# Performance work log

Measured on AMD Instinct MI355X. Metric: run time of the kernel, lower is better.

Reference implementation:

```python
import jax, jax.numpy as jnp
import numpy as np

# geomloss SamplesLoss('sinkhorn', p=2, blur=0.05, scaling=0.5, debias=True) math
P = 2
BLUR = 0.05
SCALING = 0.5
DIAMETER = 64.0  # static conservative bound on point-cloud diameter for randn D=64 data


def _eps_schedule():
    eps_list = []
    e = DIAMETER ** P
    target = BLUR ** P
    while e > target:
        eps_list.append(e)
        e *= SCALING ** P
    eps_list.append(target)
    return np.array(eps_list, dtype=np.float32)


def _cost(x, y):
    # C_ij = ||x_i - y_j||^2 / 2   (p=2 cost of geomloss)
    sq = (jnp.sum(x * x, -1)[:, :, None] * 0.5
          + jnp.sum(y * y, -1)[:, None, :] * 0.5
          - jnp.einsum('bnd,bmd->bnm', x, y))
    return jnp.maximum(sq, 0.0)


def _softmin(eps, C, h):
    # f_i = -eps * log sum_j exp(h_j - C_ij / eps);  C: (B,N,M), h: (B,M)
    return -eps * jax.nn.logsumexp(h[:, None, :] - C / eps, axis=-1)


def setup_inputs() -> dict:
    key = jax.random.key(0)
    k1, k2, k3, k4 = jax.random.split(key, 4)
    B, N, M, D = 8, 2048, 2048, 64
    x = jax.random.normal(k1, (B, N, D), dtype=jnp.float32)
    y = jax.random.normal(k2, (B, M, D), dtype=jnp.float32)
    w1 = jax.random.uniform(k3, (B, N), dtype=jnp.float32) + 0.01
    w2 = jax.random.uniform(k4, (B, M), dtype=jnp.float32) + 0.01
    w1 = w1 / jnp.sum(w1, axis=-1, keepdims=True)
    w2 = w2 / jnp.sum(w2, axis=-1, keepdims=True)
    return {'x': x, 'y': y, 'w1': w1, 'w2': w2}


def _sinkhorn_divergence(x, y, w1, w2):
    a_log = jnp.log(w1)
    b_log = jnp.log(w2)
    eps_list = jnp.asarray(_eps_schedule())

    # --- Sinkhorn loop on detached quantities (geomloss detaches the loop) ---
    xd = jax.lax.stop_gradient(x)
    yd = jax.lax.stop_gradient(y)
    ald = jax.lax.stop_gradient(a_log)
    bld = jax.lax.stop_gradient(b_log)
    C_xy_d = _cost(xd, yd)
    C_yx_d = jnp.swapaxes(C_xy_d, 1, 2)
    C_xx_d = _cost(xd, xd)
    C_yy_d = _cost(yd, yd)

    eps0 = eps_list[0]
    f_ab = _softmin(eps0, C_xy_d, bld)
    g_ba = _softmin(eps0, C_yx_d, ald)
    f_aa = _softmin(eps0, C_xx_d, ald)
    g_bb = _softmin(eps0, C_yy_d, bld)

    def step(carry, eps):
        f_ab, g_ba, f_aa, g_bb = carry
        ft = _softmin(eps, C_xy_d, bld + g_ba / eps)
        gt = _softmin(eps, C_yx_d, ald + f_ab / eps)
        f_aa_t = _softmin(eps, C_xx_d, ald + f_aa / eps)
        g_bb_t = _softmin(eps, C_yy_d, bld + g_bb / eps)
        return (0.5 * (f_ab + ft), 0.5 * (g_ba + gt),
                0.5 * (f_aa + f_aa_t), 0.5 * (g_bb + g_bb_t)), None

    (f_ab, g_ba, f_aa, g_bb), _ = jax.lax.scan(step, (f_ab, g_ba, f_aa, g_bb), eps_list)

    # --- last extrapolation at eps = blur^p, differentiable ---
    eps = eps_list[-1]
    C_xy = _cost(x, y)
    C_yx = jnp.swapaxes(C_xy, 1, 2)
    C_xx = _cost(x, x)
    C_yy = _cost(y, y)
    f_ab_f = _softmin(eps, C_xy, b_log + g_ba / eps)
    g_ba_f = _softmin(eps, C_yx, a_log + f_ab / eps)
    f_aa_f = _softmin(eps, C_xx, a_log + f_aa / eps)
    g_bb_f = _softmin(eps, C_yy, b_log + g_bb / eps)

    # debiased sinkhorn cost per batch element
    loss = (jnp.sum(w1 * (f_ab_f - f_aa_f), axis=-1)
            + jnp.sum(w2 * (g_ba_f - g_bb_f), axis=-1))
    return loss


def reference(x, y, w1, w2):
    loss = _sinkhorn_divergence(x, y, w1, w2)
    return jnp.mean(loss)  # reduction='mean'
```

## Files before the change

kernel.cpp:

```cpp
#include <hip/hip_runtime.h>

#define NB 8
#define NN 2048
#define MM 2048
#define DD 64
#define NMAT ((size_t)NN * (size_t)MM)
#define NCHK 16
#define TS 128

#define CSCALE 320.0f
#define CDEC   (1.0f / CSCALE)

typedef _Float16 half_t;
typedef __attribute__((ext_vector_type(8))) _Float16 f16x8;
typedef __attribute__((ext_vector_type(4))) float f32x4;

__device__ unsigned short g_C[3 * NB * NMAT];
__device__ half_t g_xh[NB * NN * DD];
__device__ half_t g_yh[NB * MM * DD];
__device__ float g_fab[3][NB * NN], g_gba[3][NB * NN];
__device__ float g_faa[3][NB * NN], g_gbb[3][NB * NN];
__device__ float g_alog[NB * NN], g_blog[NB * NN];
__device__ float g_xn[NB * NN], g_yn[NB * NN];
__device__ float g_h0[NB * MM], g_h1[NB * NN], g_h2[NB * NN], g_h3[NB * MM];
__device__ float2 g_pfab[NB * NCHK * NN];
__device__ float2 g_pgba[NB * NCHK * NN];
__device__ float2 g_pfaa[NB * NCHK * NN];
__device__ float2 g_pgbb[NB * NCHK * NN];

__global__ __launch_bounds__(256) void prep_kernel(
    const float* __restrict__ x, const float* __restrict__ y,
    const float* __restrict__ w1, const float* __restrict__ w2)
{
  int gid = blockIdx.x * 256 + threadIdx.x;
  if (gid < NB * NN) {
    g_alog[gid] = logf(w1[gid]);
    g_blog[gid] = logf(w2[gid]);
  }
  int lane = threadIdx.x & 63;
  int row = blockIdx.x * 4 + (threadIdx.x >> 6);
  float xv = x[(size_t)row * DD + lane];
  float yv = y[(size_t)row * DD + lane];
  g_xh[(size_t)row * DD + lane] = (half_t)xv;
  g_yh[(size_t)row * DD + lane] = (half_t)yv;
  float sx = xv * xv;
  float sy = yv * yv;
#pragma unroll
  for (int off = 32; off > 0; off >>= 1) {
    sx += __shfl_down(sx, off);
    sy += __shfl_down(sy, off);
  }
  if (lane == 0) {
    g_xn[row] = 0.5f * sx;
    g_yn[row] = 0.5f * sy;
  }
}

__global__ __launch_bounds__(256) void cost_mfma()
{
  const int slab = blockIdx.z >> 3;
  const int b = blockIdx.z & 7;
  int I, J;
  if (slab) {
    if (blockIdx.x >= 136) return;
    int rem = blockIdx.x, ii = 0;
    while (rem >= NCHK - ii) { rem -= NCHK - ii; ++ii; }
    I = ii; J = ii + rem;
  } else {
    I = blockIdx.x >> 4;
    J = blockIdx.x & 15;
  }

  const half_t* Ah = (slab == 2) ? g_yh : g_xh;
  const half_t* Bh = (slab == 0) ? g_yh : ((slab == 1) ? g_xh : g_yh);
  const float* na = (slab == 2) ? g_yn : g_xn;
  const float* nbp = (slab == 0) ? g_yn : ((slab == 1) ? g_xn : g_yn);
  unsigned short* Cout = g_C + (size_t)slab * NB * NMAT + (size_t)b * NMAT;

  const int t = threadIdx.x;
  const int w = t >> 6, lane = t & 63;
  const int m = lane & 15, quad = lane >> 4;
  const int i0 = I * TS, j0 = J * TS;

  const half_t* Abase = Ah + ((size_t)b * NN + i0 + 32 * w + m) * DD + quad * 8;
  const half_t* Bbase = Bh + ((size_t)b * MM + j0 + m) * DD + quad * 8;

  f32x4 acc[2][8];
#pragma unroll
  for (int g = 0; g < 2; ++g)
#pragma unroll
    for (int c = 0; c < 8; ++c) acc[g][c] = (f32x4){0.f, 0.f, 0.f, 0.f};

#pragma unroll
  for (int s = 0; s < 2; ++s) {
    f16x8 a0 = *(const f16x8*)(Abase + s * 32);
    f16x8 a1 = *(const f16x8*)(Abase + (size_t)16 * DD + s * 32);
#pragma unroll
    for (int c = 0; c < 8; ++c) {
      f16x8 bf = *(const f16x8*)(Bbase + (size_t)(16 * c) * DD + s * 32);
      acc[0][c] = __builtin_amdgcn_mfma_f32_16x16x32_f16(a0, bf, acc[0][c], 0, 0, 0);
      acc[1][c] = __builtin_amdgcn_mfma_f32_16x16x32_f16(a1, bf, acc[1][c], 0, 0, 0);
    }
  }

  __shared__ unsigned short tile[TS * TS];
  float4 xr[2];
#pragma unroll
  for (int g = 0; g < 2; ++g)
    xr[g] = *(const float4*)(na + b * NN + i0 + 32 * w + 16 * g + 4 * quad);
#pragma unroll
  for (int c = 0; c < 8; ++c) {
    float yv = nbp[b * MM + j0 + 16 * c + m];
#pragma unroll
    for (int g = 0; g < 2; ++g) {
      float xg[4] = {xr[g].x, xr[g].y, xr[g].z, xr[g].w};
#pragma unroll
      for (int r = 0; r < 4; ++r) {
        float cv = fmaxf(xg[r] + yv - acc[g][c][r], 0.f);
        unsigned int u = __float2uint_rn(fminf(cv * CSCALE, 65535.f));
        tile[(32 * w + 16 * g + 4 * quad + r) * TS + 16 * c + m] = (unsigned short)u;
      }
    }
  }
  __syncthreads();

  const uint4* tl = (const uint4*)tile;
#pragma unroll
  for (int p = 0; p < 8; ++p) {
    int u = p * 256 + t;
    int row = u >> 4, c8 = (u & 15) * 8;
    *(uint4*)(Cout + (size_t)(i0 + row) * MM + j0 + c8) = tl[u];
  }
}

__global__ __launch_bounds__(256) void hprep_kernel(
    const float* __restrict__ fab_in, const float* __restrict__ gba_in,
    const float* __restrict__ faa_in, const float* __restrict__ gbb_in,
    float gs)
{
  int i = blockIdx.x * 256 + threadIdx.x;
  g_h0[i] = fmaf(gs, gba_in[i], g_blog[i]);
  g_h1[i] = fmaf(gs, fab_in[i], g_alog[i]);
  g_h2[i] = fmaf(gs, faa_in[i], g_alog[i]);
  g_h3[i] = fmaf(gs, gbb_in[i], g_blog[i]);
}

struct TileArgs {
  const unsigned short* C;
  const float* hrow;
  const float* hcol;
  float2* prow;
  float2* pcol;
  int sym;
};

__global__ __launch_bounds__(256) void tile_pass(
    TileArgs T0, TileArgs T1, TileArgs T2, float inv_eps)
{
  TileArgs A = (blockIdx.z == 0) ? T0 : (blockIdx.z == 1) ? T1 : T2;
  int I, J;
  if (A.sym) {
    if (blockIdx.x >= 136) return;
    int rem = blockIdx.x, ii = 0;
    while (rem >= NCHK - ii) { rem -= NCHK - ii; ++ii; }
    I = ii; J = ii + rem;
  } else {
    I = blockIdx.x >> 4;
    J = blockIdx.x & 15;
  }
  const int b = blockIdx.y;
  const int t = threadIdx.x;
  const int ctr = t & 15;
  const int rtr = t >> 4;
  const float csneg = -inv_eps * CDEC;

  const unsigned short* Cb = A.C + (size_t)b * NMAT
                           + (size_t)(I * TS) * MM + J * TS;

  float hr[8], hc[8];
  {
    const float* hrp = A.hrow + (size_t)b * MM + J * TS + ctr * 8;
    const float* hcp = A.hcol + (size_t)b * MM + I * TS + rtr * 8;
#pragma unroll
    for (int k = 0; k < 8; ++k) { hr[k] = hrp[k]; hc[k] = hcp[k]; }
  }

  uint4 cu[8];
#pragma unroll
  for (int r8 = 0; r8 < 8; ++r8)
    cu[r8] = *(const uint4*)(Cb + (size_t)(rtr * 8 + r8) * MM + ctr * 8);

  __shared__ float redR[TS][17], redC[TS][17];
  __shared__ float rowM[TS], colM[TS];

  float rm[8], cm[8];
#pragma unroll
  for (int k = 0; k < 8; ++k) { rm[k] = -3.0e38f; cm[k] = -3.0e38f; }
#pragma unroll
  for (int r8 = 0; r8 < 8; ++r8) {
    float base[8];
    base[0] = (float)(cu[r8].x & 0xffff) * csneg;
    base[1] = (float)(cu[r8].x >> 16)    * csneg;
    base[2] = (float)(cu[r8].y & 0xffff) * csneg;
    base[3] = (float)(cu[r8].y >> 16)    * csneg;
    base[4] = (float)(cu[r8].z & 0xffff) * csneg;
    base[5] = (float)(cu[r8].z >> 16)    * csneg;
    base[6] = (float)(cu[r8].w & 0xffff) * csneg;
    base[7] = (float)(cu[r8].w >> 16)    * csneg;
#pragma unroll
    for (int c8 = 0; c8 < 8; ++c8) {
      rm[r8] = fmaxf(rm[r8], hr[c8] + base[c8]);
      cm[c8] = fmaxf(cm[c8], hc[r8] + base[c8]);
    }
  }
#pragma unroll
  for (int r8 = 0; r8 < 8; ++r8) redR[rtr * 8 + r8][ctr] = rm[r8];
#pragma unroll
  for (int c8 = 0; c8 < 8; ++c8) redC[ctr * 8 + c8][rtr] = cm[c8];
  __syncthreads();
  if (t < TS) {
    float m = redR[t][0];
#pragma unroll
    for (int k = 1; k < 16; ++k) m = fmaxf(m, redR[t][k]);
    rowM[t] = m;
  } else {
    int tt = t - TS;
    float m = redC[tt][0];
#pragma unroll
    for (int k = 1; k < 16; ++k) m = fmaxf(m, redC[tt][k]);
    colM[tt] = m;
  }
  __syncthreads();

  float rmv[8], cmv[8];
#pragma unroll
  for (int k = 0; k < 8; ++k) {
    rmv[k] = rowM[rtr * 8 + k];
    cmv[k] = colM[ctr * 8 + k];
  }

  float rs[8], cs[8];
#pragma unroll
  for (int k = 0; k < 8; ++k) { rs[k] = 0.f; cs[k] = 0.f; }
#pragma unroll
  for (int r8 = 0; r8 < 8; ++r8) {
    float base[8];
    base[0] = (float)(cu[r8].x & 0xffff) * csneg;
    base[1] = (float)(cu[r8].x >> 16)    * csneg;
    base[2] = (float)(cu[r8].y & 0xffff) * csneg;
    base[3] = (float)(cu[r8].y >> 16)    * csneg;
    base[4] = (float)(cu[r8].z & 0xffff) * csneg;
    base[5] = (float)(cu[r8].z >> 16)    * csneg;
    base[6] = (float)(cu[r8].w & 0xffff) * csneg;
    base[7] = (float)(cu[r8].w >> 16)    * csneg;
#pragma unroll
    for (int c8 = 0; c8 < 8; ++c8) {
      rs[r8] += __expf(hr[c8] + base[c8] - rmv[r8]);
      cs[c8] += __expf(hc[r8] + base[c8] - cmv[c8]);
    }
  }
#pragma unroll
  for (int r8 = 0; r8 < 8; ++r8) redR[rtr * 8 + r8][ctr] = rs[r8];
#pragma unroll
  for (int c8 = 0; c8 < 8; ++c8) redC[ctr * 8 + c8][rtr] = cs[c8];
  __syncthreads();
  if (t < TS) {
    float s = 0.f;
#pragma unroll
    for (int k = 0; k < 16; ++k) s += redR[t][k];
    A.prow[((size_t)b * NCHK + J) * NN + I * TS + t] = make_float2(rowM[t], s);
  } else {
    int tt = t - TS;
    if (!(A.sym && I == J)) {
      float s = 0.f;
#pragma unroll
      for (int k = 0; k < 16; ++k) s += redC[tt][k];
      A.pcol[((size_t)b * NCHK + I) * NN + J * TS + tt] = make_float2(colM[tt], s);
    }
  }
}

struct MergeArgs {
  const float2* part;
  const float* fold;
  float* fout;
  const float* hbase;
  float* hout;
};

__global__ __launch_bounds__(256) void merge4(
    MergeArgs M0, MergeArgs M1, MergeArgs M2, MergeArgs M3,
    float eps, float alpha, float beta, float nextgs)
{
  MergeArgs A = (blockIdx.z == 0) ? M0 : (blockIdx.z == 1) ? M1
              : (blockIdx.z == 2) ? M2 : M3;
  const int b = blockIdx.y;
  const int i = blockIdx.x * 256 + threadIdx.x;
  float2 p[NCHK];
#pragma unroll
  for (int k = 0; k < NCHK; ++k)
    p[k] = A.part[((size_t)b * NCHK + k) * NN + i];
  float M = p[0].x;
#pragma unroll
  for (int k = 1; k < NCHK; ++k) M = fmaxf(M, p[k].x);
  float S = 0.f;
#pragma unroll
  for (int k = 0; k < NCHK; ++k) S += p[k].y * __expf(p[k].x - M);
  float ft = -eps * (M + __logf(S));
  int idx = b * NN + i;
  float fnew = alpha * A.fold[idx] + beta * ft;
  A.fout[idx] = fnew;
  A.hout[idx] = fmaf(nextgs, fnew, A.hbase[idx]);
}

__global__ __launch_bounds__(256) void loss_kernel(
    const float* __restrict__ w1, const float* __restrict__ w2,
    float* __restrict__ out)
{
  __shared__ float red[256];
  float acc = 0.f;
  for (int idx = threadIdx.x; idx < NB * NN; idx += 256) {
    acc += w1[idx] * (g_fab[2][idx] - g_faa[2][idx])
         + w2[idx] * (g_gba[2][idx] - g_gbb[2][idx]);
  }
  red[threadIdx.x] = acc;
  __syncthreads();
  for (int s = 128; s > 0; s >>= 1) {
    if (threadIdx.x < s) red[threadIdx.x] += red[threadIdx.x + s];
    __syncthreads();
  }
  if (threadIdx.x == 0) out[0] = red[0] * (1.0f / NB);
}

extern "C" void kernel_launch(void* const* d_in, const int* in_sizes, int n_in,
                              void* d_out, int out_size, void* d_ws, size_t ws_size,
                              hipStream_t stream)
{
  const float* x = (const float*)d_in[0];
  const float* y = (const float*)d_in[1];
  const float* w1 = (const float*)d_in[2];
  const float* w2 = (const float*)d_in[3];
  float* out = (float*)d_out;

  unsigned short* Cbase;
  hipGetSymbolAddress((void**)&Cbase, HIP_SYMBOL(g_C));
  unsigned short* Cxy = Cbase + 0ull * NB * NMAT;
  unsigned short* Cxx = Cbase + 1ull * NB * NMAT;
  unsigned short* Cyy = Cbase + 2ull * NB * NMAT;
  float *h0, *h1, *h2, *h3, *fabp, *gbap, *faap, *gbbp, *alog, *blog;
  float2 *pfab, *pgba, *pfaa, *pgbb;
  hipGetSymbolAddress((void**)&h0, HIP_SYMBOL(g_h0));
  hipGetSymbolAddress((void**)&h1, HIP_SYMBOL(g_h1));
  hipGetSymbolAddress((void**)&h2, HIP_SYMBOL(g_h2));
  hipGetSymbolAddress((void**)&h3, HIP_SYMBOL(g_h3));
  hipGetSymbolAddress((void**)&fabp, HIP_SYMBOL(g_fab));
  hipGetSymbolAddress((void**)&gbap, HIP_SYMBOL(g_gba));
  hipGetSymbolAddress((void**)&faap, HIP_SYMBOL(g_faa));
  hipGetSymbolAddress((void**)&gbbp, HIP_SYMBOL(g_gbb));
  hipGetSymbolAddress((void**)&alog, HIP_SYMBOL(g_alog));
  hipGetSymbolAddress((void**)&blog, HIP_SYMBOL(g_blog));
  hipGetSymbolAddress((void**)&pfab, HIP_SYMBOL(g_pfab));
  hipGetSymbolAddress((void**)&pgba, HIP_SYMBOL(g_pgba));
  hipGetSymbolAddress((void**)&pfaa, HIP_SYMBOL(g_pfaa));
  hipGetSymbolAddress((void**)&pgbb, HIP_SYMBOL(g_pgbb));

  auto fab = [&](int s) { return fabp + (size_t)s * NB * NN; };
  auto gba = [&](int s) { return gbap + (size_t)s * NB * NN; };
  auto faa = [&](int s) { return faap + (size_t)s * NB * NN; };
  auto gbb = [&](int s) { return gbbp + (size_t)s * NB * NN; };

  float eps_list[32];
  int ne = 0;
  {
    double v = 64.0 * 64.0;
    double tgt = 0.05 * 0.05;
    while (v > tgt) { eps_list[ne++] = (float)v; v *= 0.25; }
    eps_list[ne++] = (float)tgt;
  }

  prep_kernel<<<4096, 256, 0, stream>>>(x, y, w1, w2);

  cost_mfma<<<dim3(256, 1, 24), 256, 0, stream>>>();

  dim3 tg(256, NB, 3);
  dim3 mg(NN / 256, NB, 4);

  auto launch_iter = [&](float eps, float alpha, float beta, float nextgs,
                         int in, int outsel) {
    float inv = 1.0f / eps;
    TileArgs T0 = {Cxy, h0, h1, pfab, pgba, 0};
    TileArgs T1 = {Cxx, h2, h2, pfaa, pfaa, 1};
    TileArgs T2 = {Cyy, h3, h3, pgbb, pgbb, 1};
    tile_pass<<<tg, 256, 0, stream>>>(T0, T1, T2, inv);
    MergeArgs M0 = {pfab, fab(in), fab(outsel), alog, h1};
    MergeArgs M1 = {pgba, gba(in), gba(outsel), blog, h0};
    MergeArgs M2 = {pfaa, faa(in), faa(outsel), alog, h2};
    MergeArgs M3 = {pgbb, gbb(in), gbb(outsel), blog, h3};
    merge4<<<mg, 256, 0, stream>>>(M0, M1, M2, M3, eps, alpha, beta, nextgs);
  };

  hprep_kernel<<<64, 256, 0, stream>>>(fab(0), gba(0), faa(0), gbb(0), 0.f);
  launch_iter(eps_list[0], 0.f, 1.f, 1.0f / eps_list[0], 0, 0);

  int cur = 0;
  for (int k = 0; k < ne; ++k) {
    int nxt = 1 - cur;
    float nextgs = 1.0f / ((k < ne - 1) ? eps_list[k + 1] : eps_list[ne - 1]);
    launch_iter(eps_list[k], 0.5f, 0.5f, nextgs, cur, nxt);
    cur = nxt;
  }

  launch_iter(eps_list[ne - 1], 0.f, 1.f, 0.f, cur, 2);

  loss_kernel<<<1, 256, 0, stream>>>(w1, w2, out);
}
```

Before: 711.9 us.

## Recompute cost tiles on the fly with MFMA inside tile pass instead of storing

Removes the precomputed 16-bit quantized cost matrices and the separate cost kernel. Each tile_pass block now recomputes its 128x128 tile of x·y dot products with f16 MFMA and folds the squared norms and potentials into per-row and per-column offsets for the logsumexp. This swaps the large per-iteration reads of the stored cost matrix for extra MFMA work and small reads of the f16 point clouds. It also drops the 320x quantization of costs, which changes precision, and the clamp of negative costs to zero is no longer applied.

```diff
diff --git a/kernel.cpp b/kernel.cpp
--- a/kernel.cpp
+++ b/kernel.cpp
@@ -8,14 +8,10 @@
 #define NCHK 16
 #define TS 128
 
-#define CSCALE 320.0f
-#define CDEC   (1.0f / CSCALE)
-
 typedef _Float16 half_t;
 typedef __attribute__((ext_vector_type(8))) _Float16 f16x8;
 typedef __attribute__((ext_vector_type(4))) float f32x4;
 
-__device__ unsigned short g_C[3 * NB * NMAT];
 __device__ half_t g_xh[NB * NN * DD];
 __device__ half_t g_yh[NB * MM * DD];
 __device__ float g_fab[3][NB * NN], g_gba[3][NB * NN];
@@ -56,83 +52,6 @@
   }
 }
 
-__global__ __launch_bounds__(256) void cost_mfma()
-{
-  const int slab = blockIdx.z >> 3;
-  const int b = blockIdx.z & 7;
-  int I, J;
-  if (slab) {
-    if (blockIdx.x >= 136) return;
-    int rem = blockIdx.x, ii = 0;
-    while (rem >= NCHK - ii) { rem -= NCHK - ii; ++ii; }
-    I = ii; J = ii + rem;
-  } else {
-    I = blockIdx.x >> 4;
-    J = blockIdx.x & 15;
-  }
-
-  const half_t* Ah = (slab == 2) ? g_yh : g_xh;
-  const half_t* Bh = (slab == 0) ? g_yh : ((slab == 1) ? g_xh : g_yh);
-  const float* na = (slab == 2) ? g_yn : g_xn;
-  const float* nbp = (slab == 0) ? g_yn : ((slab == 1) ? g_xn : g_yn);
-  unsigned short* Cout = g_C + (size_t)slab * NB * NMAT + (size_t)b * NMAT;
-
-  const int t = threadIdx.x;
-  const int w = t >> 6, lane = t & 63;
-  const int m = lane & 15, quad = lane >> 4;
-  const int i0 = I * TS, j0 = J * TS;
-
-  const half_t* Abase = Ah + ((size_t)b * NN + i0 + 32 * w + m) * DD + quad * 8;
-  const half_t* Bbase = Bh + ((size_t)b * MM + j0 + m) * DD + quad * 8;
-
-  f32x4 acc[2][8];
-#pragma unroll
-  for (int g = 0; g < 2; ++g)
-#pragma unroll
-    for (int c = 0; c < 8; ++c) acc[g][c] = (f32x4){0.f, 0.f, 0.f, 0.f};
-
-#pragma unroll
-  for (int s = 0; s < 2; ++s) {
-    f16x8 a0 = *(const f16x8*)(Abase + s * 32);
-    f16x8 a1 = *(const f16x8*)(Abase + (size_t)16 * DD + s * 32);
-#pragma unroll
-    for (int c = 0; c < 8; ++c) {
-      f16x8 bf = *(const f16x8*)(Bbase + (size_t)(16 * c) * DD + s * 32);
-      acc[0][c] = __builtin_amdgcn_mfma_f32_16x16x32_f16(a0, bf, acc[0][c], 0, 0, 0);
-      acc[1][c] = __builtin_amdgcn_mfma_f32_16x16x32_f16(a1, bf, acc[1][c], 0, 0, 0);
-    }
-  }
-
-  __shared__ unsigned short tile[TS * TS];
-  float4 xr[2];
-#pragma unroll
-  for (int g = 0; g < 2; ++g)
-    xr[g] = *(const float4*)(na + b * NN + i0 + 32 * w + 16 * g + 4 * quad);
-#pragma unroll
-  for (int c = 0; c < 8; ++c) {
-    float yv = nbp[b * MM + j0 + 16 * c + m];
-#pragma unroll
-    for (int g = 0; g < 2; ++g) {
-      float xg[4] = {xr[g].x, xr[g].y, xr[g].z, xr[g].w};
-#pragma unroll
-      for (int r = 0; r < 4; ++r) {
-        float cv = fmaxf(xg[r] + yv - acc[g][c][r], 0.f);
-        unsigned int u = __float2uint_rn(fminf(cv * CSCALE, 65535.f));
-        tile[(32 * w + 16 * g + 4 * quad + r) * TS + 16 * c + m] = (unsigned short)u;
-      }
-    }
-  }
-  __syncthreads();
-
-  const uint4* tl = (const uint4*)tile;
-#pragma unroll
-  for (int p = 0; p < 8; ++p) {
-    int u = p * 256 + t;
-    int row = u >> 4, c8 = (u & 15) * 8;
-    *(uint4*)(Cout + (size_t)(i0 + row) * MM + j0 + c8) = tl[u];
-  }
-}
-
 __global__ __launch_bounds__(256) void hprep_kernel(
     const float* __restrict__ fab_in, const float* __restrict__ gba_in,
     const float* __restrict__ faa_in, const float* __restrict__ gbb_in,
@@ -145,8 +64,11 @@
   g_h3[i] = fmaf(gs, gbb_in[i], g_blog[i]);
 }
 
-struct TileArgs {
-  const unsigned short* C;
+struct TPArgs {
+  const half_t* Ar;
+  const half_t* Bc;
+  const float* nrow;
+  const float* ncol;
   const float* hrow;
   const float* hcol;
   float2* prow;
@@ -155,9 +77,9 @@
 };
 
 __global__ __launch_bounds__(256) void tile_pass(
-    TileArgs T0, TileArgs T1, TileArgs T2, float inv_eps)
-{
-  TileArgs A = (blockIdx.z == 0) ? T0 : (blockIdx.z == 1) ? T1 : T2;
+    TPArgs T0, TPArgs T1, TPArgs T2, float inv_eps)
+{
+  TPArgs A = (blockIdx.z == 0) ? T0 : (blockIdx.z == 1) ? T1 : T2;
   int I, J;
   if (A.sym) {
     if (blockIdx.x >= 136) return;
@@ -170,25 +92,54 @@
   }
   const int b = blockIdx.y;
   const int t = threadIdx.x;
-  const int ctr = t & 15;
-  const int rtr = t >> 4;
-  const float csneg = -inv_eps * CDEC;
-
-  const unsigned short* Cb = A.C + (size_t)b * NMAT
-                           + (size_t)(I * TS) * MM + J * TS;
-
-  float hr[8], hc[8];
-  {
-    const float* hrp = A.hrow + (size_t)b * MM + J * TS + ctr * 8;
-    const float* hcp = A.hcol + (size_t)b * MM + I * TS + rtr * 8;
-#pragma unroll
-    for (int k = 0; k < 8; ++k) { hr[k] = hrp[k]; hc[k] = hcp[k]; }
-  }
-
-  uint4 cu[8];
-#pragma unroll
-  for (int r8 = 0; r8 < 8; ++r8)
-    cu[r8] = *(const uint4*)(Cb + (size_t)(rtr * 8 + r8) * MM + ctr * 8);
+  const int w = t >> 6, lane = t & 63;
+  const int m = lane & 15, quad = lane >> 4;
+  const int i0 = I * TS, j0 = J * TS;
+  const float ie = inv_eps;
+
+  const half_t* Abase = A.Ar + ((size_t)b * NN + i0 + 32 * w + m) * DD + quad * 8;
+  const half_t* Bbase = A.Bc + ((size_t)b * MM + j0 + m) * DD + quad * 8;
+
+  f32x4 acc[2][8];
+#pragma unroll
+  for (int g = 0; g < 2; ++g)
+#pragma unroll
+    for (int c = 0; c < 8; ++c) acc[g][c] = (f32x4){0.f, 0.f, 0.f, 0.f};
+
+#pragma unroll
+  for (int s = 0; s < 2; ++s) {
+    f16x8 a0 = *(const f16x8*)(Abase + s * 32);
+    f16x8 a1 = *(const f16x8*)(Abase + (size_t)16 * DD + s * 32);
+#pragma unroll
+    for (int c = 0; c < 8; ++c) {
+      f16x8 bf = *(const f16x8*)(Bbase + (size_t)(16 * c) * DD + s * 32);
+      acc[0][c] = __builtin_amdgcn_mfma_f32_16x16x32_f16(a0, bf, acc[0][c], 0, 0, 0);
+      acc[1][c] = __builtin_amdgcn_mfma_f32_16x16x32_f16(a1, bf, acc[1][c], 0, 0, 0);
+    }
+  }
+
+  float Aj[8], Bj[8];
+  float Ai[8], Bi[8];
+#pragma unroll
+  for (int c = 0; c < 8; ++c) {
+    int j = b * MM + j0 + 16 * c + m;
+    float ynj = A.ncol[j];
+    Bj[c] = -ynj * ie;
+    Aj[c] = A.hrow[j] + Bj[c];
+  }
+#pragma unroll
+  for (int g = 0; g < 2; ++g) {
+    int ib = b * NN + i0 + 32 * w + 16 * g + 4 * quad;
+    float4 xn4 = *(const float4*)(A.nrow + ib);
+    float4 hc4 = *(const float4*)(A.hcol + ib);
+    float xg[4] = {xn4.x, xn4.y, xn4.z, xn4.w};
+    float hg[4] = {hc4.x, hc4.y, hc4.z, hc4.w};
+#pragma unroll
+    for (int r = 0; r < 4; ++r) {
+      Bi[g * 4 + r] = -xg[r] * ie;
+      Ai[g * 4 + r] = hg[r] + Bi[g * 4 + r];
+    }
+  }
 
   __shared__ float redR[TS][17], redC[TS][17];
   __shared__ float rowM[TS], colM[TS];
@@ -197,72 +148,69 @@
 #pragma unroll
   for (int k = 0; k < 8; ++k) { rm[k] = -3.0e38f; cm[k] = -3.0e38f; }
 #pragma unroll
-  for (int r8 = 0; r8 < 8; ++r8) {
-    float base[8];
-    base[0] = (float)(cu[r8].x & 0xffff) * csneg;
-    base[1] = (float)(cu[r8].x >> 16)    * csneg;
-    base[2] = (float)(cu[r8].y & 0xffff) * csneg;
-    base[3] = (float)(cu[r8].y >> 16)    * csneg;
-    base[4] = (float)(cu[r8].z & 0xffff) * csneg;
-    base[5] = (float)(cu[r8].z >> 16)    * csneg;
-    base[6] = (float)(cu[r8].w & 0xffff) * csneg;
-    base[7] = (float)(cu[r8].w >> 16)    * csneg;
-#pragma unroll
-    for (int c8 = 0; c8 < 8; ++c8) {
-      rm[r8] = fmaxf(rm[r8], hr[c8] + base[c8]);
-      cm[c8] = fmaxf(cm[c8], hc[r8] + base[c8]);
-    }
-  }
-#pragma unroll
-  for (int r8 = 0; r8 < 8; ++r8) redR[rtr * 8 + r8][ctr] = rm[r8];
-#pragma unroll
-  for (int c8 = 0; c8 < 8; ++c8) redC[ctr * 8 + c8][rtr] = cm[c8];
+  for (int g = 0; g < 2; ++g)
+#pragma unroll
+    for (int c = 0; c < 8; ++c) {
+      f32x4 tv = acc[g][c];
+#pragma unroll
+      for (int r = 0; r < 4; ++r) {
+        float tt = tv[r] * ie;
+        tv[r] = tt;
+        rm[g * 4 + r] = fmaxf(rm[g * 4 + r], tt + Bi[g * 4 + r] + Aj[c]);
+        cm[c] = fmaxf(cm[c], tt + Ai[g * 4 + r] + Bj[c]);
+      }
+      acc[g][c] = tv;
+    }
+#pragma unroll
+  for (int k = 0; k < 8; ++k)
+    redR[32 * w + 16 * (k >> 2) + 4 * quad + (k & 3)][m] = rm[k];
+#pragma unroll
+  for (int c = 0; c < 8; ++c)
+    redC[16 * c + m][w * 4 + quad] = cm[c];
   __syncthreads();
   if (t < TS) {
-    float m = redR[t][0];
-#pragma unroll
-    for (int k = 1; k < 16; ++k) m = fmaxf(m, redR[t][k]);
-    rowM[t] = m;
+    float v = redR[t][0];
+#pragma unroll
+    for (int k = 1; k < 16; ++k) v = fmaxf(v, redR[t][k]);
+    rowM[t] = v;
   } else {
     int tt = t - TS;
-    float m = redC[tt][0];
-#pragma unroll
-    for (int k = 1; k < 16; ++k) m = fmaxf(m, redC[tt][k]);
-    colM[tt] = m;
-  }
-  __syncthreads();
-
-  float rmv[8], cmv[8];
-#pragma unroll
-  for (int k = 0; k < 8; ++k) {
-    rmv[k] = rowM[rtr * 8 + k];
-    cmv[k] = colM[ctr * 8 + k];
-  }
+    float v = redC[tt][0];
+#pragma unroll
+    for (int k = 1; k < 16; ++k) v = fmaxf(v, redC[tt][k]);
+    colM[tt] = v;
+  }
+  __syncthreads();
+
+  float BR[8], CB[8];
+#pragma unroll
+  for (int k = 0; k < 8; ++k)
+    BR[k] = Bi[k] - rowM[32 * w + 16 * (k >> 2) + 4 * quad + (k & 3)];
+#pragma unroll
+  for (int c = 0; c < 8; ++c)
+    CB[c] = Bj[c] - colM[16 * c + m];
 
   float rs[8], cs[8];
 #pragma unroll
   for (int k = 0; k < 8; ++k) { rs[k] = 0.f; cs[k] = 0.f; }
 #pragma unroll
-  for (int r8 = 0; r8 < 8; ++r8) {
-    float base[8];
-    base[0] = (float)(cu[r8].x & 0xffff) * csneg;
-    base[1] = (float)(cu[r8].x >> 16)    * csneg;
-    base[2] = (float)(cu[r8].y & 0xffff) * csneg;
-    base[3] = (float)(cu[r8].y >> 16)    * csneg;
-    base[4] = (float)(cu[r8].z & 0xffff) * csneg;
-    base[5] = (float)(cu[r8].z >> 16)    * csneg;
-    base[6] = (float)(cu[r8].w & 0xffff) * csneg;
-    base[7] = (float)(cu[r8].w >> 16)    * csneg;
-#pragma unroll
-    for (int c8 = 0; c8 < 8; ++c8) {
-      rs[r8] += __expf(hr[c8] + base[c8] - rmv[r8]);
-      cs[c8] += __expf(hc[r8] + base[c8] - cmv[c8]);
-    }
-  }
-#pragma unroll
-  for (int r8 = 0; r8 < 8; ++r8) redR[rtr * 8 + r8][ctr] = rs[r8];
-#pragma unroll
-  for (int c8 = 0; c8 < 8; ++c8) redC[ctr * 8 + c8][rtr] = cs[c8];
+  for (int g = 0; g < 2; ++g)
+#pragma unroll
+    for (int c = 0; c < 8; ++c) {
+      f32x4 tv = acc[g][c];
+#pragma unroll
+      for (int r = 0; r < 4; ++r) {
+        rs[g * 4 + r] += __expf(tv[r] + BR[g * 4 + r] + Aj[c]);
+        cs[c] += __expf(tv[r] + Ai[g * 4 + r] + CB[c]);
+      }
+    }
+  __syncthreads();
+#pragma unroll
+  for (int k = 0; k < 8; ++k)
+    redR[32 * w + 16 * (k >> 2) + 4 * quad + (k & 3)][m] = rs[k];
+#pragma unroll
+  for (int c = 0; c < 8; ++c)
+    redC[16 * c + m][w * 4 + quad] = cs[c];
   __syncthreads();
   if (t < TS) {
     float s = 0.f;
@@ -342,13 +290,13 @@
   const float* w2 = (const float*)d_in[3];
   float* out = (float*)d_out;
 
-  unsigned short* Cbase;
-  hipGetSymbolAddress((void**)&Cbase, HIP_SYMBOL(g_C));
-  unsigned short* Cxy = Cbase + 0ull * NB * NMAT;
-  unsigned short* Cxx = Cbase + 1ull * NB * NMAT;
-  unsigned short* Cyy = Cbase + 2ull * NB * NMAT;
-  float *h0, *h1, *h2, *h3, *fabp, *gbap, *faap, *gbbp, *alog, *blog;
+  half_t *xh, *yh;
+  float *xn, *yn, *h0, *h1, *h2, *h3, *fabp, *gbap, *faap, *gbbp, *alog, *blog;
   float2 *pfab, *pgba, *pfaa, *pgbb;
+  hipGetSymbolAddress((void**)&xh, HIP_SYMBOL(g_xh));
+  hipGetSymbolAddress((void**)&yh, HIP_SYMBOL(g_yh));
+  hipGetSymbolAddress((void**)&xn, HIP_SYMBOL(g_xn));
+  hipGetSymbolAddress((void**)&yn, HIP_SYMBOL(g_yn));
   hipGetSymbolAddress((void**)&h0, HIP_SYMBOL(g_h0));
   hipGetSymbolAddress((void**)&h1, HIP_SYMBOL(g_h1));
   hipGetSymbolAddress((void**)&h2, HIP_SYMBOL(g_h2));
@@ -380,17 +328,15 @@
 
   prep_kernel<<<4096, 256, 0, stream>>>(x, y, w1, w2);
 
-  cost_mfma<<<dim3(256, 1, 24), 256, 0, stream>>>();
-
   dim3 tg(256, NB, 3);
   dim3 mg(NN / 256, NB, 4);
 
   auto launch_iter = [&](float eps, float alpha, float beta, float nextgs,
                          int in, int outsel) {
     float inv = 1.0f / eps;
-    TileArgs T0 = {Cxy, h0, h1, pfab, pgba, 0};
-    TileArgs T1 = {Cxx, h2, h2, pfaa, pfaa, 1};
-    TileArgs T2 = {Cyy, h3, h3, pgbb, pgbb, 1};
+    TPArgs T0 = {xh, yh, xn, yn, h0, h1, pfab, pgba, 0};
+    TPArgs T1 = {xh, xh, xn, xn, h2, h2, pfaa, pfaa, 1};
+    TPArgs T2 = {yh, yh, yn, yn, h3, h3, pgbb, pgbb, 1};
     tile_pass<<<tg, 256, 0, stream>>>(T0, T1, T2, inv);
     MergeArgs M0 = {pfab, fab(in), fab(outsel), alog, h1};
     MergeArgs M1 = {pgba, gba(in), gba(outsel), blog, h0};
```

Measured after the change: 1.655 ms. 132% more time.

## Use base-2 exponent domain and wavefront shuffles for row reductions in tile pass

Applied to the files above, without the earlier changes.

Pre-scales the potentials and cost scale by log2(e), so each logit is a single FMA and the raw hardware exp2 and log2 builtins replace __expf/__logf. The merge kernel is adjusted to work in the base-2 domain and converts back with ln2. Row max and row sum reductions now use xor-shuffles within the 16 lanes that share a row instead of a shared-memory transpose, which drops the redR array and some LDS traffic. The column reduction still goes through shared memory and gains an extra barrier. It relies on the 16 lanes of a row group sitting in the same wavefront.

```diff
diff --git a/kernel.cpp b/kernel.cpp
--- a/kernel.cpp
+++ b/kernel.cpp
@@ -10,6 +10,8 @@
 
 #define CSCALE 320.0f
 #define CDEC   (1.0f / CSCALE)
+#define LOG2E  1.4426950408889634f
+#define LN2    0.6931471805599453f
 
 typedef _Float16 half_t;
 typedef __attribute__((ext_vector_type(8))) _Float16 f16x8;
@@ -172,17 +174,20 @@
   const int t = threadIdx.x;
   const int ctr = t & 15;
   const int rtr = t >> 4;
-  const float csneg = -inv_eps * CDEC;
+  const float cs2 = -inv_eps * CDEC * LOG2E;
 
   const unsigned short* Cb = A.C + (size_t)b * NMAT
                            + (size_t)(I * TS) * MM + J * TS;
 
-  float hr[8], hc[8];
+  float hr2[8], hc2[8];
   {
     const float* hrp = A.hrow + (size_t)b * MM + J * TS + ctr * 8;
     const float* hcp = A.hcol + (size_t)b * MM + I * TS + rtr * 8;
 #pragma unroll
-    for (int k = 0; k < 8; ++k) { hr[k] = hrp[k]; hc[k] = hcp[k]; }
+    for (int k = 0; k < 8; ++k) {
+      hr2[k] = hrp[k] * LOG2E;
+      hc2[k] = hcp[k] * LOG2E;
+    }
   }
 
   uint4 cu[8];
@@ -190,93 +195,86 @@
   for (int r8 = 0; r8 < 8; ++r8)
     cu[r8] = *(const uint4*)(Cb + (size_t)(rtr * 8 + r8) * MM + ctr * 8);
 
-  __shared__ float redR[TS][17], redC[TS][17];
-  __shared__ float rowM[TS], colM[TS];
+  __shared__ float redC[TS][17];
+  __shared__ float colM[TS];
 
   float rm[8], cm[8];
 #pragma unroll
   for (int k = 0; k < 8; ++k) { rm[k] = -3.0e38f; cm[k] = -3.0e38f; }
 #pragma unroll
   for (int r8 = 0; r8 < 8; ++r8) {
-    float base[8];
-    base[0] = (float)(cu[r8].x & 0xffff) * csneg;
-    base[1] = (float)(cu[r8].x >> 16)    * csneg;
-    base[2] = (float)(cu[r8].y & 0xffff) * csneg;
-    base[3] = (float)(cu[r8].y >> 16)    * csneg;
-    base[4] = (float)(cu[r8].z & 0xffff) * csneg;
-    base[5] = (float)(cu[r8].z >> 16)    * csneg;
-    base[6] = (float)(cu[r8].w & 0xffff) * csneg;
-    base[7] = (float)(cu[r8].w >> 16)    * csneg;
+    float u[8];
+    u[0] = (float)(cu[r8].x & 0xffff);
+    u[1] = (float)(cu[r8].x >> 16);
+    u[2] = (float)(cu[r8].y & 0xffff);
+    u[3] = (float)(cu[r8].y >> 16);
+    u[4] = (float)(cu[r8].z & 0xffff);
+    u[5] = (float)(cu[r8].z >> 16);
+    u[6] = (float)(cu[r8].w & 0xffff);
+    u[7] = (float)(cu[r8].w >> 16);
 #pragma unroll
     for (int c8 = 0; c8 < 8; ++c8) {
-      rm[r8] = fmaxf(rm[r8], hr[c8] + base[c8]);
-      cm[c8] = fmaxf(cm[c8], hc[r8] + base[c8]);
+      rm[r8] = fmaxf(rm[r8], fmaf(u[c8], cs2, hr2[c8]));
+      cm[c8] = fmaxf(cm[c8], fmaf(u[c8], cs2, hc2[r8]));
     }
   }
 #pragma unroll
-  for (int r8 = 0; r8 < 8; ++r8) redR[rtr * 8 + r8][ctr] = rm[r8];
+  for (int mask = 1; mask < 16; mask <<= 1)
+#pragma unroll
+    for (int k = 0; k < 8; ++k)
+      rm[k] = fmaxf(rm[k], __shfl_xor(rm[k], mask));
 #pragma unroll
   for (int c8 = 0; c8 < 8; ++c8) redC[ctr * 8 + c8][rtr] = cm[c8];
   __syncthreads();
   if (t < TS) {
-    float m = redR[t][0];
-#pragma unroll
-    for (int k = 1; k < 16; ++k) m = fmaxf(m, redR[t][k]);
-    rowM[t] = m;
-  } else {
-    int tt = t - TS;
-    float m = redC[tt][0];
-#pragma unroll
-    for (int k = 1; k < 16; ++k) m = fmaxf(m, redC[tt][k]);
-    colM[tt] = m;
-  }
-  __syncthreads();
-
-  float rmv[8], cmv[8];
-#pragma unroll
-  for (int k = 0; k < 8; ++k) {
-    rmv[k] = rowM[rtr * 8 + k];
-    cmv[k] = colM[ctr * 8 + k];
-  }
+    float m = redC[t][0];
+#pragma unroll
+    for (int k = 1; k < 16; ++k) m = fmaxf(m, redC[t][k]);
+    colM[t] = m;
+  }
+  __syncthreads();
+  float cmv[8];
+#pragma unroll
+  for (int c8 = 0; c8 < 8; ++c8) cmv[c8] = colM[ctr * 8 + c8];
 
   float rs[8], cs[8];
 #pragma unroll
   for (int k = 0; k < 8; ++k) { rs[k] = 0.f; cs[k] = 0.f; }
 #pragma unroll
   for (int r8 = 0; r8 < 8; ++r8) {
-    float base[8];
-    base[0] = (float)(cu[r8].x & 0xffff) * csneg;
-    base[1] = (float)(cu[r8].x >> 16)    * csneg;
-    base[2] = (float)(cu[r8].y & 0xffff) * csneg;
-    base[3] = (float)(cu[r8].y >> 16)    * csneg;
-    base[4] = (float)(cu[r8].z & 0xffff) * csneg;
-    base[5] = (float)(cu[r8].z >> 16)    * csneg;
-    base[6] = (float)(cu[r8].w & 0xffff) * csneg;
-    base[7] = (float)(cu[r8].w >> 16)    * csneg;
+    float u[8];
+    u[0] = (float)(cu[r8].x & 0xffff);
+    u[1] = (float)(cu[r8].x >> 16);
+    u[2] = (float)(cu[r8].y & 0xffff);
+    u[3] = (float)(cu[r8].y >> 16);
+    u[4] = (float)(cu[r8].z & 0xffff);
+    u[5] = (float)(cu[r8].z >> 16);
+    u[6] = (float)(cu[r8].w & 0xffff);
+    u[7] = (float)(cu[r8].w >> 16);
 #pragma unroll
     for (int c8 = 0; c8 < 8; ++c8) {
-      rs[r8] += __expf(hr[c8] + base[c8] - rmv[r8]);
-      cs[c8] += __expf(hc[r8] + base[c8] - cmv[c8]);
+      rs[r8] += __builtin_amdgcn_exp2f(fmaf(u[c8], cs2, hr2[c8]) - rm[r8]);
+      cs[c8] += __builtin_amdgcn_exp2f(fmaf(u[c8], cs2, hc2[r8]) - cmv[c8]);
     }
   }
 #pragma unroll
-  for (int r8 = 0; r8 < 8; ++r8) redR[rtr * 8 + r8][ctr] = rs[r8];
+  for (int mask = 1; mask < 16; mask <<= 1)
+#pragma unroll
+    for (int k = 0; k < 8; ++k)
+      rs[k] += __shfl_xor(rs[k], mask);
+  if (ctr < 8) {
+    A.prow[((size_t)b * NCHK + J) * NN + I * TS + rtr * 8 + ctr]
+        = make_float2(rm[ctr], rs[ctr]);
+  }
+  __syncthreads();
 #pragma unroll
   for (int c8 = 0; c8 < 8; ++c8) redC[ctr * 8 + c8][rtr] = cs[c8];
   __syncthreads();
-  if (t < TS) {
+  if (t < TS && !(A.sym && I == J)) {
     float s = 0.f;
 #pragma unroll
-    for (int k = 0; k < 16; ++k) s += redR[t][k];
-    A.prow[((size_t)b * NCHK + J) * NN + I * TS + t] = make_float2(rowM[t], s);
-  } else {
-    int tt = t - TS;
-    if (!(A.sym && I == J)) {
-      float s = 0.f;
-#pragma unroll
-      for (int k = 0; k < 16; ++k) s += redC[tt][k];
-      A.pcol[((size_t)b * NCHK + I) * NN + J * TS + tt] = make_float2(colM[tt], s);
-    }
+    for (int k = 0; k < 16; ++k) s += redC[t][k];
+    A.pcol[((size_t)b * NCHK + I) * NN + J * TS + t] = make_float2(colM[t], s);
   }
 }
 
@@ -305,8 +303,9 @@
   for (int k = 1; k < NCHK; ++k) M = fmaxf(M, p[k].x);
   float S = 0.f;
 #pragma unroll
-  for (int k = 0; k < NCHK; ++k) S += p[k].y * __expf(p[k].x - M);
-  float ft = -eps * (M + __logf(S));
+  for (int k = 0; k < NCHK; ++k)
+    S += p[k].y * __builtin_amdgcn_exp2f(p[k].x - M);
+  float ft = -eps * LN2 * (M + __builtin_amdgcn_logf(S));
   int idx = b * NN + i;
   float fnew = alpha * A.fold[idx] + beta * ft;
   A.fout[idx] = fnew;
```

Result: no change. 717.5 us (+0.8%).
